# Optimization experiments

Measured on AMD Instinct MI355X. Metric: run time of the kernel, lower is better.

The kernel has to match this reference:

```python
import jax, jax.numpy as jnp
import numpy as np

N, C, D = 65536, 256, 1024
ALPHA = 1.0   # alpha init arg
GAMMA = 0.01  # gamma init arg


def setup_inputs() -> dict:
    key = jax.random.key(0)
    k1, k2, k3, k4 = jax.random.split(key, 4)
    features = jax.random.normal(k1, (N, D), dtype=jnp.float32)
    labels = jax.random.randint(k2, (N, 1), 0, C, dtype=jnp.int64)
    cluster = jax.random.normal(k3, (C, D), dtype=jnp.float32)
    class_weight = jax.random.uniform(k4, (C,), dtype=jnp.float32)
    return {"features": features, "labels": labels, "cluster": cluster,
            "class_weight": class_weight}


def reference(features, labels, cluster, class_weight):
    # features: [N, D], labels: [N, 1], cluster: [C, D], class_weight: [C]
    lab = labels[:, 0]                                  # [N]
    ci = cluster[lab]                                   # gather centers [N, D]
    diff = features - ci                                # [N, D]
    nume = jnp.sum(diff * diff, axis=-1)                # ||x_i - c_{l_i}||^2, [N]

    # denom_i = sum_j ||c_j - c_{l_i}||^2 + alpha  (pairwise via gram, [C,C])
    sq = jnp.sum(cluster * cluster, axis=-1)            # [C]
    pair = jnp.maximum(sq[:, None] + sq[None, :] - 2.0 * cluster @ cluster.T, 0.0)
    per_class_denom = jnp.sum(pair, axis=1)             # [C]
    denom = per_class_denom[lab] + ALPHA                # [N]

    loss = (nume / denom)[:, None]                      # [N, 1] (matches TF output)

    # centroid update: delta_c[l] = sum_{i: l_i=l} w_l * (x_i - c_l) / denom_i
    contrib = (class_weight[lab] / denom)[:, None] * diff   # [N, D]
    weighted_delta_c = jax.ops.segment_sum(contrib, lab, num_segments=C)  # [C, D]
    new_cluster = cluster - GAMMA * weighted_delta_c    # assign_sub semantics

    return loss, new_cluster
```

## Files before the change

kernel.cpp:

```cpp
#include <hip/hip_runtime.h>

#define N_SAMPLES 65536
#define C_CLASSES 256
#define D_DIM     1024
#define ALPHA_C   1.0f
#define GAMMA_C   0.01f
#define LCAP      1024
#define NW        16

__global__ __launch_bounds__(1024, 1) void fused_kernel(
    const float* __restrict__ features,
    const int*   __restrict__ labels, int lab_stride,
    const float* __restrict__ cluster,
    const float* __restrict__ cls_w,
    float* __restrict__ loss_out,
    float* __restrict__ out_cluster)
{
    __shared__ int   list_[LCAP];
    __shared__ int   s_cnt;
    __shared__ float s_denom;
    __shared__ alignas(16) float cc[D_DIM];
    __shared__ float sqv[C_CLASSES];
    __shared__ float dotv[C_CLASSES];
    __shared__ alignas(16) float comb[NW][D_DIM];

    const int c = blockIdx.x;
    const int t = threadIdx.x;
    const int w = t >> 6, lane = t & 63;

    if (t == 0) s_cnt = 0;
    if (t < 256) ((float4*)cc)[t] = ((const float4*)(cluster + (size_t)c * D_DIM))[t];
    __syncthreads();

#define COMPACT4(m0, m1, m2, m3, s0)                                         \
    {                                                                        \
        unsigned long long b0 = __ballot(m0), b1 = __ballot(m1);             \
        unsigned long long b2 = __ballot(m2), b3 = __ballot(m3);             \
        int tot = __popcll(b0) + __popcll(b1) + __popcll(b2) + __popcll(b3); \
        if (tot) {                                                           \
            int bb = 0;                                                      \
            if (lane == 0) bb = atomicAdd(&s_cnt, tot);                      \
            bb = __shfl(bb, 0, 64);                                          \
            unsigned long long lm = (1ull << lane) - 1ull;                   \
            int p = bb + __popcll(b0 & lm) + __popcll(b1 & lm)               \
                       + __popcll(b2 & lm) + __popcll(b3 & lm);              \
            if (m0) { if (p < LCAP) list_[p] = (s0);     ++p; }              \
            if (m1) { if (p < LCAP) list_[p] = (s0) + 1; ++p; }              \
            if (m2) { if (p < LCAP) list_[p] = (s0) + 2; ++p; }              \
            if (m3) { if (p < LCAP) list_[p] = (s0) + 3; ++p; }              \
        }                                                                    \
    }

    if (lab_stride == 2) {
        const int4* lab4 = (const int4*)labels;
        for (int iter = 0; iter < 16; ++iter) {
            int chunk = iter * NW + w;
            int s0 = chunk * 256 + lane * 4;
            int4 v0 = lab4[(s0 >> 1)];
            int4 v1 = lab4[(s0 >> 1) + 1];
            COMPACT4(v0.x == c, v0.z == c, v1.x == c, v1.z == c, s0);
        }
    } else {
        const int4* lab4 = (const int4*)labels;
        for (int iter = 0; iter < 16; ++iter) {
            int chunk = iter * NW + w;
            int s0 = chunk * 256 + lane * 4;
            int4 v = lab4[s0 >> 2];
            COMPACT4(v.x == c, v.y == c, v.z == c, v.w == c, s0);
        }
    }
#undef COMPACT4
    __syncthreads();
    const int cnt = (s_cnt > LCAP) ? LCAP : s_cnt;
    const float4* cc4 = (const float4*)cc;

    for (int r = w; r < C_CLASSES; r += NW) {
        const float4* row = (const float4*)(cluster + (size_t)r * D_DIM);
        float sq = 0.f, dt = 0.f;
#pragma unroll
        for (int j = 0; j < 4; ++j) {
            float4 v = row[j * 64 + lane];
            float4 a = cc4[j * 64 + lane];
            sq += v.x * v.x + v.y * v.y + v.z * v.z + v.w * v.w;
            dt += v.x * a.x + v.y * a.y + v.z * a.z + v.w * a.w;
        }
#pragma unroll
        for (int m = 32; m >= 1; m >>= 1) {
            sq += __shfl_xor(sq, m, 64);
            dt += __shfl_xor(dt, m, 64);
        }
        if (lane == 0) { sqv[r] = sq; dotv[r] = dt; }
    }
    __syncthreads();

    if (t < 64) {
        float sqc = sqv[c];
        float s = 0.f;
#pragma unroll
        for (int jj = 0; jj < 4; ++jj) {
            int j = jj * 64 + lane;
            float p = sqc + sqv[j] - 2.f * dotv[j];
            s += (p > 0.f ? p : 0.f);
        }
#pragma unroll
        for (int m = 32; m >= 1; m >>= 1) s += __shfl_xor(s, m, 64);
        if (lane == 0) s_denom = s + ALPHA_C;
    }
    __syncthreads();
    const float inv_dnm = 1.0f / s_denom;

    float4 ck[4];
#pragma unroll
    for (int j = 0; j < 4; ++j) ck[j] = cc4[j * 64 + lane];

    float4 dsum[4];
#pragma unroll
    for (int j = 0; j < 4; ++j) dsum[j] = make_float4(0.f, 0.f, 0.f, 0.f);

    int niter = (cnt > w) ? ((cnt - w - 1) / NW + 1) : 0;

#define LOADROW(buf, idx)                                                    \
    {                                                                        \
        const float4* f_ = (const float4*)(features + (size_t)(idx) * D_DIM);\
        _Pragma("unroll")                                                    \
        for (int j = 0; j < 4; ++j) buf[j] = f_[j * 64 + lane];              \
    }
#define COMPUTE(buf, idx)                                                    \
    {                                                                        \
        float nume = 0.f;                                                    \
        _Pragma("unroll")                                                    \
        for (int j = 0; j < 4; ++j) {                                        \
            float dx = buf[j].x - ck[j].x, dy = buf[j].y - ck[j].y;          \
            float dz = buf[j].z - ck[j].z, dw = buf[j].w - ck[j].w;          \
            dsum[j].x += dx; dsum[j].y += dy;                                \
            dsum[j].z += dz; dsum[j].w += dw;                                \
            nume += dx * dx + dy * dy + dz * dz + dw * dw;                   \
        }                                                                    \
        _Pragma("unroll")                                                    \
        for (int m = 32; m >= 1; m >>= 1) nume += __shfl_xor(nume, m, 64);   \
        if (lane == 0) loss_out[idx] = nume * inv_dnm;                       \
    }

    float4 bufA[4], bufB[4];
    int ia = (0 < niter) ? list_[w] : -1;
    int ib = (1 < niter) ? list_[w + NW] : -1;
    if (ia >= 0) LOADROW(bufA, ia);
    int n = 0;
    while (n + 1 < niter) {
        LOADROW(bufB, ib);
        int ic = (n + 2 < niter) ? list_[w + (n + 2) * NW] : -1;
        COMPUTE(bufA, ia);
        if (ic >= 0) LOADROW(bufA, ic);
        int id = (n + 3 < niter) ? list_[w + (n + 3) * NW] : -1;
        COMPUTE(bufB, ib);
        ia = ic; ib = id; n += 2;
    }
    if (n < niter) COMPUTE(bufA, ia);
#undef LOADROW
#undef COMPUTE

    {
        float4* cwv = (float4*)comb[w];
#pragma unroll
        for (int j = 0; j < 4; ++j) cwv[j * 64 + lane] = dsum[j];
    }
    __syncthreads();
    if (t < 256) {
        float sc_ = GAMMA_C * cls_w[c] * inv_dnm;
        float4 s = make_float4(0.f, 0.f, 0.f, 0.f);
#pragma unroll
        for (int r = 0; r < NW; ++r) {
            float4 u = ((const float4*)comb[r])[t];
            s.x += u.x; s.y += u.y; s.z += u.z; s.w += u.w;
        }
        float4 cv = cc4[t];
        float4 o;
        o.x = cv.x - sc_ * s.x;
        o.y = cv.y - sc_ * s.y;
        o.z = cv.z - sc_ * s.z;
        o.w = cv.w - sc_ * s.w;
        ((float4*)(out_cluster + (size_t)c * D_DIM))[t] = o;
    }
}

extern "C" void kernel_launch(void* const* d_in, const int* in_sizes, int n_in,
                              void* d_out, int out_size, void* d_ws, size_t ws_size,
                              hipStream_t stream) {
    const float* features = (const float*)d_in[0];
    const int*   labels   = (const int*)d_in[1];
    const float* cluster  = (const float*)d_in[2];
    const float* cls_w    = (const float*)d_in[3];
    int lab_stride = in_sizes[1] / N_SAMPLES;
    if (lab_stride < 1) lab_stride = 1;

    float* loss_out    = (float*)d_out;
    float* out_cluster = (float*)d_out + N_SAMPLES;

    fused_kernel<<<C_CLASSES, 1024, 0, stream>>>(features, labels, lab_stride,
                                                 cluster, cls_w, loss_out, out_cluster);
}
```

Baseline: 65.50 us.

## Precompute cluster norms and column sums; split classes across two blocks

```diff
diff --git a/kernel.cpp b/kernel.cpp
--- a/kernel.cpp
+++ b/kernel.cpp
@@ -5,14 +5,62 @@
 #define D_DIM     1024
 #define ALPHA_C   1.0f
 #define GAMMA_C   0.01f
-#define LCAP      1024
+#define LCAP      512
 #define NW        16
 
-__global__ __launch_bounds__(1024, 1) void fused_kernel(
+__global__ __launch_bounds__(256) void prep_kernel(
+    const float* __restrict__ cluster,
+    float* __restrict__ sqv_g,
+    float* __restrict__ T_g,
+    float* __restrict__ out_cluster)
+{
+    int bid = blockIdx.x, t = threadIdx.x;
+    int w = t >> 6, lane = t & 63;
+
+    if (bid < 64) {
+        int c = bid * 4 + w;
+        const float4* row = (const float4*)(cluster + (size_t)c * D_DIM);
+        float sq = 0.f;
+#pragma unroll
+        for (int j = 0; j < 4; ++j) {
+            float4 v = row[j * 64 + lane];
+            sq += v.x * v.x + v.y * v.y + v.z * v.z + v.w * v.w;
+        }
+#pragma unroll
+        for (int m = 32; m >= 1; m >>= 1) sq += __shfl_xor(sq, m, 64);
+        if (lane == 0) sqv_g[c] = sq;
+        return;
+    }
+    if (bid < 80) {
+        __shared__ float part[4][64];
+        int dimbase = (bid - 64) * 64;
+        const float* base = cluster + dimbase + lane;
+        float s = 0.f;
+#pragma unroll 4
+        for (int i = 0; i < 64; ++i) {
+            int r = w * 64 + i;
+            s += base[(size_t)r * D_DIM];
+        }
+        part[w][lane] = s;
+        __syncthreads();
+        if (w == 0)
+            T_g[dimbase + lane] = part[0][lane] + part[1][lane] +
+                                  part[2][lane] + part[3][lane];
+        return;
+    }
+    {
+        int b = bid - 80;
+        ((float4*)out_cluster)[b * 256 + t] = make_float4(0.f, 0.f, 0.f, 0.f);
+    }
+}
+
+__global__ __launch_bounds__(1024, 8) void main_kernel(
     const float* __restrict__ features,
     const int*   __restrict__ labels, int lab_stride,
     const float* __restrict__ cluster,
     const float* __restrict__ cls_w,
+    const float* __restrict__ sqv_g,
+    const float* __restrict__ T_g,
     float* __restrict__ loss_out,
     float* __restrict__ out_cluster)
 {
@@ -20,17 +68,17 @@
     __shared__ int   s_cnt;
     __shared__ float s_denom;
     __shared__ alignas(16) float cc[D_DIM];
-    __shared__ float sqv[C_CLASSES];
-    __shared__ float dotv[C_CLASSES];
     __shared__ alignas(16) float comb[NW][D_DIM];
 
-    const int c = blockIdx.x;
+    const int bid = blockIdx.x;
+    const int c = bid >> 1, h = bid & 1;
     const int t = threadIdx.x;
     const int w = t >> 6, lane = t & 63;
 
     if (t == 0) s_cnt = 0;
     if (t < 256) ((float4*)cc)[t] = ((const float4*)(cluster + (size_t)c * D_DIM))[t];
     __syncthreads();
+    const float4* cc4 = (const float4*)cc;
 
 #define COMPACT4(m0, m1, m2, m3, s0)                                         \
     {                                                                        \
@@ -51,10 +99,10 @@
         }                                                                    \
     }
 
+    const int ch0 = h * 128, ch1 = ch0 + 128;
     if (lab_stride == 2) {
         const int4* lab4 = (const int4*)labels;
-        for (int iter = 0; iter < 16; ++iter) {
-            int chunk = iter * NW + w;
+        for (int chunk = ch0 + w; chunk < ch1; chunk += NW) {
             int s0 = chunk * 256 + lane * 4;
             int4 v0 = lab4[(s0 >> 1)];
             int4 v1 = lab4[(s0 >> 1) + 1];
@@ -62,8 +110,7 @@
         }
     } else {
         const int4* lab4 = (const int4*)labels;
-        for (int iter = 0; iter < 16; ++iter) {
-            int chunk = iter * NW + w;
+        for (int chunk = ch0 + w; chunk < ch1; chunk += NW) {
             int s0 = chunk * 256 + lane * 4;
             int4 v = lab4[s0 >> 2];
             COMPACT4(v.x == c, v.y == c, v.z == c, v.w == c, s0);
@@ -72,39 +119,25 @@
 #undef COMPACT4
     __syncthreads();
     const int cnt = (s_cnt > LCAP) ? LCAP : s_cnt;
-    const float4* cc4 = (const float4*)cc;
-
-    for (int r = w; r < C_CLASSES; r += NW) {
-        const float4* row = (const float4*)(cluster + (size_t)r * D_DIM);
-        float sq = 0.f, dt = 0.f;
+
+    if (w == 0) {
+        const float4* T4 = (const float4*)T_g;
+        float dt = 0.f;
 #pragma unroll
         for (int j = 0; j < 4; ++j) {
-            float4 v = row[j * 64 + lane];
-            float4 a = cc4[j * 64 + lane];
-            sq += v.x * v.x + v.y * v.y + v.z * v.z + v.w * v.w;
-            dt += v.x * a.x + v.y * a.y + v.z * a.z + v.w * a.w;
-        }
+            float4 tv = T4[j * 64 + lane];
+            float4 av = cc4[j * 64 + lane];
+            dt += tv.x * av.x + tv.y * av.y + tv.z * av.z + tv.w * av.w;
+        }
+        float4 sv = ((const float4*)sqv_g)[lane];
+        float S = sv.x + sv.y + sv.z + sv.w;
 #pragma unroll
         for (int m = 32; m >= 1; m >>= 1) {
-            sq += __shfl_xor(sq, m, 64);
             dt += __shfl_xor(dt, m, 64);
-        }
-        if (lane == 0) { sqv[r] = sq; dotv[r] = dt; }
-    }
-    __syncthreads();
-
-    if (t < 64) {
-        float sqc = sqv[c];
-        float s = 0.f;
-#pragma unroll
-        for (int jj = 0; jj < 4; ++jj) {
-            int j = jj * 64 + lane;
-            float p = sqc + sqv[j] - 2.f * dotv[j];
-            s += (p > 0.f ? p : 0.f);
-        }
-#pragma unroll
-        for (int m = 32; m >= 1; m >>= 1) s += __shfl_xor(s, m, 64);
-        if (lane == 0) s_denom = s + ALPHA_C;
+            S  += __shfl_xor(S,  m, 64);
+        }
+        if (lane == 0)
+            s_denom = 256.f * sqv_g[c] + S - 2.f * dt + ALPHA_C;
     }
     __syncthreads();
     const float inv_dnm = 1.0f / s_denom;
@@ -174,12 +207,15 @@
             s.x += u.x; s.y += u.y; s.z += u.z; s.w += u.w;
         }
         float4 cv = cc4[t];
-        float4 o;
-        o.x = cv.x - sc_ * s.x;
-        o.y = cv.y - sc_ * s.y;
-        o.z = cv.z - sc_ * s.z;
-        o.w = cv.w - sc_ * s.w;
-        ((float4*)(out_cluster + (size_t)c * D_DIM))[t] = o;
+        float ax = (h == 0 ? cv.x : 0.f) - sc_ * s.x;
+        float ay = (h == 0 ? cv.y : 0.f) - sc_ * s.y;
+        float az = (h == 0 ? cv.z : 0.f) - sc_ * s.z;
+        float aw = (h == 0 ? cv.w : 0.f) - sc_ * s.w;
+        float* outc = out_cluster + (size_t)c * D_DIM + 4 * t;
+        atomicAdd(outc + 0, ax);
+        atomicAdd(outc + 1, ay);
+        atomicAdd(outc + 2, az);
+        atomicAdd(outc + 3, aw);
     }
 }
 
@@ -196,6 +232,12 @@
     float* loss_out    = (float*)d_out;
     float* out_cluster = (float*)d_out + N_SAMPLES;
 
-    fused_kernel<<<C_CLASSES, 1024, 0, stream>>>(features, labels, lab_stride,
-                                                 cluster, cls_w, loss_out, out_cluster);
+    char* ws = (char*)d_ws;
+    float* sqv_g = (float*)(ws);
+    float* T_g   = (float*)(ws + 4096);
+
+    prep_kernel<<<336, 256, 0, stream>>>(cluster, sqv_g, T_g, out_cluster);
+    main_kernel<<<2 * C_CLASSES, 1024, 0, stream>>>(features, labels, lab_stride,
+                                                    cluster, cls_w, sqv_g, T_g,
+                                                    loss_out, out_cluster);
 }
```

Result: slower. 199.7 us (+204.8%).
